# Performance work log

Hardware: AMD Instinct MI355X
Metric: run time of the kernel (lower is better)

The kernel has to match this reference:

```python
import jax, jax.numpy as jnp
import numpy as np

B, S, HID = 2, 2048, 2048
NH, NKV, HD = 16, 8, 256
EPS = 1e-6
SCALE = 256 ** -0.5  # query_pre_attn_scalar ** -0.5


def setup_inputs() -> dict:
    key = jax.random.key(0)
    k1, k2, k3 = jax.random.split(key, 3)
    hidden_states = jax.random.normal(k1, (B, S, HID), dtype=jnp.float32)
    w_qkv = jax.random.normal(k2, (HID, (NH + 2 * NKV) * HD), dtype=jnp.float32) * 0.02
    w_o = jax.random.normal(k3, (NH * HD, HID), dtype=jnp.float32) * 0.02
    q_norm_w = jnp.zeros((HD,), dtype=jnp.float32)  # Gemma RMSNorm uses (1 + w)
    k_norm_w = jnp.zeros((HD,), dtype=jnp.float32)
    # Real rotary tables: inv_freq over half dim, emb = concat(freqs, freqs)
    inv_freq = 1.0 / (10000.0 ** (jnp.arange(0, HD, 2, dtype=jnp.float32) / HD))
    pos = jnp.arange(S, dtype=jnp.float32)
    freqs = pos[:, None] * inv_freq[None, :]            # [S, HD/2]
    emb = jnp.concatenate([freqs, freqs], axis=-1)       # [S, HD]
    cos = jnp.broadcast_to(jnp.cos(emb)[None], (B, S, HD))
    sin = jnp.broadcast_to(jnp.sin(emb)[None], (B, S, HD))
    return {"hidden_states": hidden_states, "cos": cos, "sin": sin,
            "w_qkv": w_qkv, "w_o": w_o, "q_norm_w": q_norm_w, "k_norm_w": k_norm_w}


def _rms_norm(x, w):
    # Gemma3RMSNorm: fp32 rms, scale by (1 + w)
    xf = x.astype(jnp.float32)
    var = jnp.mean(xf * xf, axis=-1, keepdims=True)
    out = xf * jax.lax.rsqrt(var + EPS) * (1.0 + w.astype(jnp.float32))
    return out.astype(x.dtype)


def _rotate_half(x):
    x1, x2 = jnp.split(x, 2, axis=-1)
    return jnp.concatenate([-x2, x1], axis=-1)


def reference(hidden_states, cos, sin, w_qkv, w_o, q_norm_w, k_norm_w):
    qkv = jnp.einsum("bsh,hf->bsf", hidden_states, w_qkv)
    q, k, v = jnp.split(qkv, [NH * HD, NH * HD + NKV * HD], axis=-1)
    q = q.reshape(B, S, NH, HD).transpose(0, 2, 1, 3)    # [b, nh, s, d]
    k = k.reshape(B, S, NKV, HD).transpose(0, 2, 1, 3)   # [b, nkv, s, d]
    v = v.reshape(B, S, NKV, HD).transpose(0, 2, 1, 3)
    q = _rms_norm(q, q_norm_w)
    k = _rms_norm(k, k_norm_w)
    c = cos[:, None, :, :]  # broadcast over heads
    s = sin[:, None, :, :]
    q = q * c + _rotate_half(q) * s
    k = k * c + _rotate_half(k) * s
    n_rep = NH // NKV
    k = jnp.repeat(k, n_rep, axis=1)  # GQA expand: [b, nh, s, d]
    v = jnp.repeat(v, n_rep, axis=1)
    scores = jnp.einsum("bhqd,bhkd->bhqk", q, k) * SCALE
    attn = jax.nn.softmax(scores, axis=-1)
    out = jnp.einsum("bhqk,bhkd->bhqd", attn, v)
    out = out.transpose(0, 2, 1, 3).reshape(B, S, NH * HD)
    return jnp.einsum("bsf,fh->bsh", out, w_o)
```

## Files before the change

kernel.cpp:

```cpp
#include <hip/hip_runtime.h>
#include <stdint.h>

typedef __attribute__((ext_vector_type(8))) short short8;
typedef __attribute__((ext_vector_type(4))) short short4v;
typedef __attribute__((ext_vector_type(4))) float f32x4;

#define GLOAD16(gp, lp) __builtin_amdgcn_global_load_lds( \
    (__attribute__((address_space(1))) void*)(gp),        \
    (__attribute__((address_space(3))) void*)(lp), 16, 0, 0)

__device__ __forceinline__ unsigned short f2bf(float f) {
    union { float f; unsigned u; } v; v.f = f;
    unsigned u = v.u + 0x7fffu + ((v.u >> 16) & 1u);
    return (unsigned short)(u >> 16);
}
__device__ __forceinline__ float bf2f(short s) {
    union { unsigned u; float f; } v;
    v.u = ((unsigned)(unsigned short)s) << 16;
    return v.f;
}

__global__ __launch_bounds__(256) void cvt_f32_bf16(const float* __restrict__ in,
                                                    short* __restrict__ out) {
    const int i = (blockIdx.x * 256 + threadIdx.x) * 4;
    const float4 v = *(const float4*)(in + i);
    short4v o;
    o[0] = (short)f2bf(v.x); o[1] = (short)f2bf(v.y);
    o[2] = (short)f2bf(v.z); o[3] = (short)f2bf(v.w);
    *(short4v*)(out + i) = o;
}

__global__ __launch_bounds__(256) void transpose_cvt(const float* __restrict__ in,
                                                     short* __restrict__ out,
                                                     int R, int C) {
    __shared__ float tile[64 * 65];
    const int t = threadIdx.x;
    const int r0 = blockIdx.y * 64, c0 = blockIdx.x * 64;
    const int rl = t >> 4, cl4 = (t & 15) * 4;
#pragma unroll
    for (int rep = 0; rep < 4; rep++) {
        const int r = rep * 16 + rl;
        const float4 v = *(const float4*)(in + (long)(r0 + r) * C + c0 + cl4);
        tile[r * 65 + cl4 + 0] = v.x;
        tile[r * 65 + cl4 + 1] = v.y;
        tile[r * 65 + cl4 + 2] = v.z;
        tile[r * 65 + cl4 + 3] = v.w;
    }
    __syncthreads();
#pragma unroll
    for (int rep = 0; rep < 4; rep++) {
        const int cc = rep * 16 + rl;
        short4v o;
#pragma unroll
        for (int j = 0; j < 4; j++) o[j] = (short)f2bf(tile[(cl4 + j) * 65 + cc]);
        *(short4v*)(out + (long)(c0 + cc) * R + r0 + cl4) = o;
    }
}

__global__ __launch_bounds__(256) void vtrans(const short* __restrict__ QKV,
                                              short* __restrict__ Vt) {
    __shared__ short tile[64 * 72];
    const int t = threadIdx.x;
    const int s0 = blockIdx.x * 64, d0 = blockIdx.y * 64;
    const int hb = blockIdx.z >> 1, b = blockIdx.z & 1;
    const short* src = QKV + ((long)(24 + hb) * 4096 + b * 2048) * 256;
    short* dst = Vt + (long)blockIdx.z * 256 * 2048;
#pragma unroll
    for (int p = 0; p < 2; p++) {
        const int c = p * 256 + t;
        const int r = c >> 3, col8 = (c & 7) * 8;
        *(short8*)(tile + r * 72 + col8) = *(const short8*)(src + (long)(s0 + r) * 256 + d0 + col8);
    }
    __syncthreads();
#pragma unroll
    for (int p = 0; p < 2; p++) {
        const int c = p * 256 + t;
        const int dr = c >> 3, sc8 = (c & 7) * 8;
        short8 o;
#pragma unroll
        for (int j = 0; j < 8; j++) o[j] = tile[(sc8 + j) * 72 + dr];
        *(short8*)(dst + (long)(d0 + dr) * 2048 + s0 + sc8) = o;
    }
}

template<int N, int K, int OUTMODE>
__global__ __launch_bounds__(256) void gemm_nt(const short* __restrict__ A,
                                               const short* __restrict__ Bt,
                                               void* __restrict__ Cv) {
    __shared__ __align__(16) short Al[128 * 32];
    __shared__ __align__(16) short Bl[128 * 32];
    const int t = threadIdx.x;
    const int lane = t & 63, w = t >> 6;
    const int quad = lane >> 4, l16 = lane & 15;
    const int wr = w >> 1, wc = w & 1;
    const long m0 = (long)blockIdx.y * 128, n0 = (long)blockIdx.x * 128;

    const short* Ag0 = A + (m0 + (t >> 2)) * K + (t & 3) * 8;
    const short* Bg0 = Bt + (n0 + (t >> 2)) * K + (t & 3) * 8;

    f32x4 acc[4][4] = {};

    for (int k0 = 0; k0 < K; k0 += 32) {
        __syncthreads();
        GLOAD16(Ag0 + k0,            Al + t * 8);
        GLOAD16(Ag0 + 64 * K + k0,   Al + (t + 256) * 8);
        GLOAD16(Bg0 + k0,            Bl + t * 8);
        GLOAD16(Bg0 + 64 * K + k0,   Bl + (t + 256) * 8);
        __syncthreads();
        short8 af[4], bfr[4];
#pragma unroll
        for (int i = 0; i < 4; i++)
            af[i] = *(const short8*)(Al + (wr * 64 + i * 16 + l16) * 32 + quad * 8);
#pragma unroll
        for (int i = 0; i < 4; i++)
            bfr[i] = *(const short8*)(Bl + (wc * 64 + i * 16 + l16) * 32 + quad * 8);
#pragma unroll
        for (int mi = 0; mi < 4; mi++)
#pragma unroll
            for (int ni = 0; ni < 4; ni++)
                acc[mi][ni] = __builtin_amdgcn_mfma_f32_16x16x32_bf16(af[mi], bfr[ni], acc[mi][ni], 0, 0, 0);
    }

    const long crow = m0 + wr * 64 + quad * 4;
    const long ccol = n0 + wc * 64 + l16;
    if constexpr (OUTMODE == 0) {
        float* C = (float*)Cv;
#pragma unroll
        for (int mi = 0; mi < 4; mi++)
#pragma unroll
            for (int ni = 0; ni < 4; ni++)
#pragma unroll
                for (int r = 0; r < 4; r++)
                    C[(crow + mi * 16 + r) * N + ccol + ni * 16] = acc[mi][ni][r];
    } else {
        short* C = (short*)Cv;
#pragma unroll
        for (int mi = 0; mi < 4; mi++)
#pragma unroll
            for (int ni = 0; ni < 4; ni++)
#pragma unroll
                for (int r = 0; r < 4; r++) {
                    const long m = crow + mi * 16 + r;
                    const long f = ccol + ni * 16;
                    C[(f >> 8) * 1048576 + m * 256 + (f & 255)] = (short)f2bf(acc[mi][ni][r]);
                }
    }
}

__global__ __launch_bounds__(256) void prep_qk(short* __restrict__ QKV,
                                               const float* __restrict__ cosp,
                                               const float* __restrict__ sinp,
                                               const float* __restrict__ qw,
                                               const float* __restrict__ kw) {
    const int t = threadIdx.x, w = t >> 6, lane = t & 63;
    const int d4 = lane * 4;
    const float sgn = (lane < 32) ? -1.0f : 1.0f;
#pragma unroll
    for (int i = 0; i < 4; i++) {
        const int g = blockIdx.x * 16 + w * 4 + i;
        const int u = g >> 12, m = g & 4095;
        short* rowp = QKV + (long)g * 256;
        const short4v raw = *(const short4v*)(rowp + d4);
        float x[4];
#pragma unroll
        for (int j = 0; j < 4; j++) x[j] = bf2f(raw[j]);
        float ss = x[0]*x[0] + x[1]*x[1] + x[2]*x[2] + x[3]*x[3];
#pragma unroll
        for (int msk = 1; msk < 64; msk <<= 1) ss += __shfl_xor(ss, msk, 64);
        const float rinv = rsqrtf(ss * (1.0f / 256.0f) + 1e-6f);
        const float4 wv = *(const float4*)(((u < 16) ? qw : kw) + d4);
        const float wa[4] = {wv.x, wv.y, wv.z, wv.w};
        const float4 cv = *(const float4*)(cosp + (long)m * 256 + d4);
        const float4 sv = *(const float4*)(sinp + (long)m * 256 + d4);
        const float ca[4] = {cv.x, cv.y, cv.z, cv.w};
        const float sa[4] = {sv.x, sv.y, sv.z, sv.w};
        float n[4];
#pragma unroll
        for (int j = 0; j < 4; j++) n[j] = x[j] * rinv * (1.0f + wa[j]);
        const float scale = (u < 16) ? 0.0625f : 1.0f;
        short4v ov;
#pragma unroll
        for (int j = 0; j < 4; j++) {
            const float p = __shfl_xor(n[j], 32, 64);
            ov[j] = (short)f2bf((n[j] * ca[j] + sgn * p * sa[j]) * scale);
        }
        *(short4v*)(rowp + d4) = ov;
    }
}

__global__ __launch_bounds__(512, 2) void attn(const short* __restrict__ QKV,
                                               const short* __restrict__ Vt,
                                               short* __restrict__ O) {
    __shared__ __align__(16) short Kl[2][64 * 256];
    __shared__ __align__(16) short Vl[256 * 64];
    __shared__ __align__(16) short Pl[128 * 72];
    __shared__ __align__(16) float Alp[128];
    __shared__ __align__(16) float Ll[128];

    const int t = threadIdx.x, w = t >> 6, lane = t & 63;
    const int quad = lane >> 4, l16 = lane & 15;
    const int q0 = blockIdx.x * 128, h = blockIdx.y, b = blockIdx.z;
    const int kh = h >> 1;
    const short* Qp = QKV + ((long)h * 4096 + b * 2048 + q0) * 256;
    const short* Kp = QKV + ((long)(16 + kh) * 4096 + b * 2048) * 256;
    const short* Vp = Vt + (long)(kh * 2 + b) * 256 * 2048;

    short8 qf[8];
#pragma unroll
    for (int ks = 0; ks < 8; ks++)
        qf[ks] = *(const short8*)(Qp + (w * 16 + l16) * 256 + ks * 32 + quad * 8);

    f32x4 acc[4][4] = {};
    float mi_[4], li_[4];
#pragma unroll
    for (int r = 0; r < 4; r++) { mi_[r] = -1e30f; li_[r] = 0.0f; }

    const int qh = w >> 2, dstr = (w & 3) * 64;

#pragma unroll
    for (int i = 0; i < 4; i++) {
        const int c = i * 512 + t;
        const int rK = c >> 5, j = c & 31;
        GLOAD16(Kp + (long)rK * 256 + (j ^ (rK & 31)) * 8, Kl[0] + c * 8);
    }

    for (int kt = 0; kt < 32; kt++) {
        const int k0 = kt * 64;
        __syncthreads();

#pragma unroll
        for (int i = 0; i < 4; i++) {
            const int c = i * 512 + t;
            const int dV = c >> 3, j = c & 7;
            GLOAD16(Vp + (long)dV * 2048 + k0 + (j ^ (dV & 7)) * 8, Vl + c * 8);
        }
        const int kn = ((kt + 1) & 31) * 64;
#pragma unroll
        for (int i = 0; i < 4; i++) {
            const int c = i * 512 + t;
            const int rK = c >> 5, j = c & 31;
            GLOAD16(Kp + (long)(kn + rK) * 256 + (j ^ (rK & 31)) * 8, Kl[(kt + 1) & 1] + c * 8);
        }

        const short* Kb = Kl[kt & 1];
        f32x4 sc[4] = {};
#pragma unroll
        for (int ct = 0; ct < 4; ct++) {
            const int rowK = ct * 16 + l16;
#pragma unroll
            for (int ks = 0; ks < 8; ks++) {
                const int dc = (ks * 4 + quad) ^ (rowK & 31);
                const short8 kf = *(const short8*)(Kb + rowK * 256 + dc * 8);
                sc[ct] = __builtin_amdgcn_mfma_f32_16x16x32_bf16(qf[ks], kf, sc[ct], 0, 0, 0);
            }
        }

        float al[4];
#pragma unroll
        for (int r = 0; r < 4; r++) {
            float v = fmaxf(fmaxf(sc[0][r], sc[1][r]), fmaxf(sc[2][r], sc[3][r]));
            v = fmaxf(v, __shfl_xor(v, 1, 64));
            v = fmaxf(v, __shfl_xor(v, 2, 64));
            v = fmaxf(v, __shfl_xor(v, 4, 64));
            v = fmaxf(v, __shfl_xor(v, 8, 64));
            const float mn = fmaxf(mi_[r], v);
            al[r] = __expf(mi_[r] - mn);
            mi_[r] = mn;
        }
        float rs[4] = {0.0f, 0.0f, 0.0f, 0.0f};
#pragma unroll
        for (int ct = 0; ct < 4; ct++) {
#pragma unroll
            for (int r = 0; r < 4; r++) {
                const float p = __expf(sc[ct][r] - mi_[r]);
                rs[r] += p;
                Pl[(w * 16 + quad * 4 + r) * 72 + ct * 16 + l16] = (short)f2bf(p);
            }
        }
#pragma unroll
        for (int r = 0; r < 4; r++) {
            float v = rs[r];
            v += __shfl_xor(v, 1, 64);
            v += __shfl_xor(v, 2, 64);
            v += __shfl_xor(v, 4, 64);
            v += __shfl_xor(v, 8, 64);
            li_[r] = li_[r] * al[r] + v;
        }
        if (l16 == 0) {
#pragma unroll
            for (int r = 0; r < 4; r++) Alp[w * 16 + quad * 4 + r] = al[r];
        }
        __syncthreads();

#pragma unroll
        for (int mi2 = 0; mi2 < 4; mi2++) {
            const float4 av = *(const float4*)(Alp + qh * 64 + mi2 * 16 + quad * 4);
            const float aa[4] = {av.x, av.y, av.z, av.w};
#pragma unroll
            for (int ni = 0; ni < 4; ni++)
#pragma unroll
                for (int r = 0; r < 4; r++)
                    acc[mi2][ni][r] *= aa[r];
        }
#pragma unroll
        for (int k2 = 0; k2 < 2; k2++) {
            short8 pf[4];
#pragma unroll
            for (int mi2 = 0; mi2 < 4; mi2++)
                pf[mi2] = *(const short8*)(Pl + (qh * 64 + mi2 * 16 + l16) * 72 + k2 * 32 + quad * 8);
#pragma unroll
            for (int ni = 0; ni < 4; ni++) {
                const int dV = dstr + ni * 16 + l16;
                const int dc = (k2 * 4 + quad) ^ (dV & 7);
                const short8 vf = *(const short8*)(Vl + dV * 64 + dc * 8);
#pragma unroll
                for (int mi2 = 0; mi2 < 4; mi2++)
                    acc[mi2][ni] = __builtin_amdgcn_mfma_f32_16x16x32_bf16(pf[mi2], vf, acc[mi2][ni], 0, 0, 0);
            }
        }
    }

    if (l16 == 0) {
#pragma unroll
        for (int r = 0; r < 4; r++) Ll[w * 16 + quad * 4 + r] = li_[r];
    }
    __syncthreads();

    short* Op = O + (long)(b * 2048 + q0 + qh * 64) * 4096 + h * 256 + dstr;
#pragma unroll
    for (int mi2 = 0; mi2 < 4; mi2++) {
        const float4 lv = *(const float4*)(Ll + qh * 64 + mi2 * 16 + quad * 4);
        const float inv[4] = {1.0f / lv.x, 1.0f / lv.y, 1.0f / lv.z, 1.0f / lv.w};
#pragma unroll
        for (int ni = 0; ni < 4; ni++)
#pragma unroll
            for (int r = 0; r < 4; r++)
                Op[(long)(mi2 * 16 + quad * 4 + r) * 4096 + ni * 16 + l16] =
                    (short)f2bf(acc[mi2][ni][r] * inv[r]);
    }
}

extern "C" void kernel_launch(void* const* d_in, const int* in_sizes, int n_in,
                              void* d_out, int out_size, void* d_ws, size_t ws_size,
                              hipStream_t stream) {
    const float* hs   = (const float*)d_in[0];
    const float* cosp = (const float*)d_in[1];
    const float* sinp = (const float*)d_in[2];
    const float* wqkv = (const float*)d_in[3];
    const float* wo   = (const float*)d_in[4];
    const float* qnw  = (const float*)d_in[5];
    const float* knw  = (const float*)d_in[6];
    float* out = (float*)d_out;

    short* poolA  = (short*)d_ws;
    short* Xb     = poolA;
    short* Wqkv_t = poolA + (size_t)4096 * 2048;
    short* QKV    = poolA + (size_t)4096 * 2048 + (size_t)8192 * 2048;
    short* Vt     = poolA;
    short* Ob     = poolA + (size_t)16 * 256 * 2048;
    short* Wo_t   = QKV;

    cvt_f32_bf16<<<8192, 256, 0, stream>>>(hs, Xb);
    transpose_cvt<<<dim3(128, 32), 256, 0, stream>>>(wqkv, Wqkv_t, 2048, 8192);
    gemm_nt<8192, 2048, 2><<<dim3(64, 32), 256, 0, stream>>>(Xb, Wqkv_t, (void*)QKV);
    prep_qk<<<6144, 256, 0, stream>>>(QKV, cosp, sinp, qnw, knw);
    vtrans<<<dim3(32, 4, 16), 256, 0, stream>>>(QKV, Vt);
    attn<<<dim3(16, 16, 2), 512, 0, stream>>>(QKV, Vt, Ob);
    transpose_cvt<<<dim3(32, 64), 256, 0, stream>>>(wo, Wo_t, 4096, 2048);
    gemm_nt<2048, 4096, 0><<<dim3(16, 32), 256, 0, stream>>>(Ob, Wo_t, (void*)out);
}
```

Measured before the change: 674.1 us.

## Warp-specialize attention into QK-softmax and PV warps with software pipelining

Splits the eight waves of the attention block into four score waves, which compute QK^T and softmax for 32 query rows each, and four PV waves, which accumulate P·V for all 128 rows over a 64-column slice of the head dimension. V is double-buffered and the PV step runs one tile behind the score step, so the two phases overlap across iterations. This is meant to hide softmax latency behind MFMA work. The cost is a larger accumulator (128 fp32 values per lane in the PV waves), which adds register pressure and may reduce occupancy under launch_bounds(512,2), plus an extra 32 KB of LDS and one extra loop iteration.

```diff
diff --git a/kernel.cpp b/kernel.cpp
--- a/kernel.cpp
+++ b/kernel.cpp
@@ -192,7 +192,7 @@
                                                const short* __restrict__ Vt,
                                                short* __restrict__ O) {
     __shared__ __align__(16) short Kl[2][64 * 256];
-    __shared__ __align__(16) short Vl[256 * 64];
+    __shared__ __align__(16) short Vl[2][256 * 64];
     __shared__ __align__(16) short Pl[128 * 72];
     __shared__ __align__(16) float Alp[128];
     __shared__ __align__(16) float Ll[128];
@@ -205,17 +205,32 @@
     const short* Kp = QKV + ((long)(16 + kh) * 4096 + b * 2048) * 256;
     const short* Vp = Vt + (long)(kh * 2 + b) * 256 * 2048;
 
-    short8 qf[8];
-#pragma unroll
-    for (int ks = 0; ks < 8; ks++)
-        qf[ks] = *(const short8*)(Qp + (w * 16 + l16) * 256 + ks * 32 + quad * 8);
-
-    f32x4 acc[4][4] = {};
-    float mi_[4], li_[4];
-#pragma unroll
-    for (int r = 0; r < 4; r++) { mi_[r] = -1e30f; li_[r] = 0.0f; }
-
-    const int qh = w >> 2, dstr = (w & 3) * 64;
+    const bool is_s = (w < 4);
+    const int qb = w * 32;
+    const int dstr = (w - 4) * 64;
+
+    short8 qf[2][8];
+    f32x4 sc[2][4];
+    float mi_[2][4], li_[2][4];
+    f32x4 acc[8][4];
+
+    if (is_s) {
+#pragma unroll
+        for (int g = 0; g < 2; g++)
+#pragma unroll
+            for (int ks = 0; ks < 8; ks++)
+                qf[g][ks] = *(const short8*)(Qp + (qb + g * 16 + l16) * 256 + ks * 32 + quad * 8);
+#pragma unroll
+        for (int g = 0; g < 2; g++)
+#pragma unroll
+            for (int r = 0; r < 4; r++) { mi_[g][r] = -1e30f; li_[g][r] = 0.0f; }
+    } else {
+#pragma unroll
+        for (int qt = 0; qt < 8; qt++)
+#pragma unroll
+            for (int dt = 0; dt < 4; dt++)
+                acc[qt][dt] = (f32x4){0.f, 0.f, 0.f, 0.f};
+    }
 
 #pragma unroll
     for (int i = 0; i < 4; i++) {
@@ -224,119 +239,141 @@
         GLOAD16(Kp + (long)rK * 256 + (j ^ (rK & 31)) * 8, Kl[0] + c * 8);
     }
 
-    for (int kt = 0; kt < 32; kt++) {
-        const int k0 = kt * 64;
+    for (int kt = 0; kt <= 32; kt++) {
         __syncthreads();
 
-#pragma unroll
-        for (int i = 0; i < 4; i++) {
-            const int c = i * 512 + t;
-            const int dV = c >> 3, j = c & 7;
-            GLOAD16(Vp + (long)dV * 2048 + k0 + (j ^ (dV & 7)) * 8, Vl + c * 8);
-        }
-        const int kn = ((kt + 1) & 31) * 64;
-#pragma unroll
-        for (int i = 0; i < 4; i++) {
-            const int c = i * 512 + t;
-            const int rK = c >> 5, j = c & 31;
-            GLOAD16(Kp + (long)(kn + rK) * 256 + (j ^ (rK & 31)) * 8, Kl[(kt + 1) & 1] + c * 8);
-        }
-
-        const short* Kb = Kl[kt & 1];
-        f32x4 sc[4] = {};
-#pragma unroll
-        for (int ct = 0; ct < 4; ct++) {
-            const int rowK = ct * 16 + l16;
-#pragma unroll
-            for (int ks = 0; ks < 8; ks++) {
-                const int dc = (ks * 4 + quad) ^ (rowK & 31);
-                const short8 kf = *(const short8*)(Kb + rowK * 256 + dc * 8);
-                sc[ct] = __builtin_amdgcn_mfma_f32_16x16x32_bf16(qf[ks], kf, sc[ct], 0, 0, 0);
-            }
-        }
-
-        float al[4];
-#pragma unroll
-        for (int r = 0; r < 4; r++) {
-            float v = fmaxf(fmaxf(sc[0][r], sc[1][r]), fmaxf(sc[2][r], sc[3][r]));
-            v = fmaxf(v, __shfl_xor(v, 1, 64));
-            v = fmaxf(v, __shfl_xor(v, 2, 64));
-            v = fmaxf(v, __shfl_xor(v, 4, 64));
-            v = fmaxf(v, __shfl_xor(v, 8, 64));
-            const float mn = fmaxf(mi_[r], v);
-            al[r] = __expf(mi_[r] - mn);
-            mi_[r] = mn;
-        }
-        float rs[4] = {0.0f, 0.0f, 0.0f, 0.0f};
-#pragma unroll
-        for (int ct = 0; ct < 4; ct++) {
-#pragma unroll
-            for (int r = 0; r < 4; r++) {
-                const float p = __expf(sc[ct][r] - mi_[r]);
-                rs[r] += p;
-                Pl[(w * 16 + quad * 4 + r) * 72 + ct * 16 + l16] = (short)f2bf(p);
-            }
-        }
-#pragma unroll
-        for (int r = 0; r < 4; r++) {
-            float v = rs[r];
-            v += __shfl_xor(v, 1, 64);
-            v += __shfl_xor(v, 2, 64);
-            v += __shfl_xor(v, 4, 64);
-            v += __shfl_xor(v, 8, 64);
-            li_[r] = li_[r] * al[r] + v;
-        }
-        if (l16 == 0) {
-#pragma unroll
-            for (int r = 0; r < 4; r++) Alp[w * 16 + quad * 4 + r] = al[r];
-        }
+        if (kt < 32) {
+            const int k0 = kt * 64;
+#pragma unroll
+            for (int i = 0; i < 4; i++) {
+                const int c = i * 512 + t;
+                const int dV = c >> 3, j = c & 7;
+                GLOAD16(Vp + (long)dV * 2048 + k0 + (j ^ (dV & 7)) * 8, Vl[kt & 1] + c * 8);
+            }
+        }
+        if (kt + 1 < 32) {
+            const int kn = (kt + 1) * 64;
+#pragma unroll
+            for (int i = 0; i < 4; i++) {
+                const int c = i * 512 + t;
+                const int rK = c >> 5, j = c & 31;
+                GLOAD16(Kp + (long)(kn + rK) * 256 + (j ^ (rK & 31)) * 8, Kl[(kt + 1) & 1] + c * 8);
+            }
+        }
+
+        if (is_s) {
+            if (kt < 32) {
+                const short* Kb = Kl[kt & 1];
+#pragma unroll
+                for (int g = 0; g < 2; g++)
+#pragma unroll
+                    for (int ct = 0; ct < 4; ct++) sc[g][ct] = (f32x4){0.f, 0.f, 0.f, 0.f};
+#pragma unroll
+                for (int ct = 0; ct < 4; ct++) {
+                    const int rowK = ct * 16 + l16;
+#pragma unroll
+                    for (int ks = 0; ks < 8; ks++) {
+                        const int dc = (ks * 4 + quad) ^ (rowK & 31);
+                        const short8 kf = *(const short8*)(Kb + rowK * 256 + dc * 8);
+                        sc[0][ct] = __builtin_amdgcn_mfma_f32_16x16x32_bf16(qf[0][ks], kf, sc[0][ct], 0, 0, 0);
+                        sc[1][ct] = __builtin_amdgcn_mfma_f32_16x16x32_bf16(qf[1][ks], kf, sc[1][ct], 0, 0, 0);
+                    }
+                }
+            }
+        } else if (kt >= 1) {
+            const short* Vb = Vl[(kt - 1) & 1];
+#pragma unroll
+            for (int qt = 0; qt < 8; qt++) {
+                const float4 av = *(const float4*)(Alp + qt * 16 + quad * 4);
+                const float aa[4] = {av.x, av.y, av.z, av.w};
+#pragma unroll
+                for (int dt = 0; dt < 4; dt++)
+#pragma unroll
+                    for (int r = 0; r < 4; r++) acc[qt][dt][r] *= aa[r];
+            }
+#pragma unroll
+            for (int k2 = 0; k2 < 2; k2++) {
+                short8 vf[4];
+#pragma unroll
+                for (int dt = 0; dt < 4; dt++) {
+                    const int dV = dstr + dt * 16 + l16;
+                    const int dc = (k2 * 4 + quad) ^ (dV & 7);
+                    vf[dt] = *(const short8*)(Vb + dV * 64 + dc * 8);
+                }
+#pragma unroll
+                for (int qt = 0; qt < 8; qt++) {
+                    const short8 pf = *(const short8*)(Pl + (qt * 16 + l16) * 72 + k2 * 32 + quad * 8);
+#pragma unroll
+                    for (int dt = 0; dt < 4; dt++)
+                        acc[qt][dt] = __builtin_amdgcn_mfma_f32_16x16x32_bf16(pf, vf[dt], acc[qt][dt], 0, 0, 0);
+                }
+            }
+        }
+
         __syncthreads();
 
-#pragma unroll
-        for (int mi2 = 0; mi2 < 4; mi2++) {
-            const float4 av = *(const float4*)(Alp + qh * 64 + mi2 * 16 + quad * 4);
-            const float aa[4] = {av.x, av.y, av.z, av.w};
-#pragma unroll
-            for (int ni = 0; ni < 4; ni++)
+        if (is_s && kt < 32) {
+#pragma unroll
+            for (int g = 0; g < 2; g++) {
+                float al[4];
+#pragma unroll
+                for (int r = 0; r < 4; r++) {
+                    float v = fmaxf(fmaxf(sc[g][0][r], sc[g][1][r]), fmaxf(sc[g][2][r], sc[g][3][r]));
+                    v = fmaxf(v, __shfl_xor(v, 1, 64));
+                    v = fmaxf(v, __shfl_xor(v, 2, 64));
+                    v = fmaxf(v, __shfl_xor(v, 4, 64));
+                    v = fmaxf(v, __shfl_xor(v, 8, 64));
+                    const float mn = fmaxf(mi_[g][r], v);
+                    al[r] = __expf(mi_[g][r] - mn);
+                    mi_[g][r] = mn;
+                }
+                float rs[4] = {0.f, 0.f, 0.f, 0.f};
+#pragma unroll
+                for (int ct = 0; ct < 4; ct++) {
+#pragma unroll
+                    for (int r = 0; r < 4; r++) {
+                        const float p = __expf(sc[g][ct][r] - mi_[g][r]);
+                        rs[r] += p;
+                        Pl[(qb + g * 16 + quad * 4 + r) * 72 + ct * 16 + l16] = (short)f2bf(p);
+                    }
+                }
+#pragma unroll
+                for (int r = 0; r < 4; r++) {
+                    float v = rs[r];
+                    v += __shfl_xor(v, 1, 64);
+                    v += __shfl_xor(v, 2, 64);
+                    v += __shfl_xor(v, 4, 64);
+                    v += __shfl_xor(v, 8, 64);
+                    li_[g][r] = li_[g][r] * al[r] + v;
+                }
+                if (l16 == 0) {
+#pragma unroll
+                    for (int r = 0; r < 4; r++) Alp[qb + g * 16 + quad * 4 + r] = al[r];
+                }
+            }
+        }
+    }
+
+    if (is_s && l16 == 0) {
+#pragma unroll
+        for (int g = 0; g < 2; g++)
+#pragma unroll
+            for (int r = 0; r < 4; r++) Ll[qb + g * 16 + quad * 4 + r] = li_[g][r];
+    }
+    __syncthreads();
+    if (!is_s) {
+        short* Op = O + (long)(b * 2048 + q0) * 4096 + h * 256 + dstr;
+#pragma unroll
+        for (int qt = 0; qt < 8; qt++) {
+            const float4 lv = *(const float4*)(Ll + qt * 16 + quad * 4);
+            const float inv[4] = {1.0f / lv.x, 1.0f / lv.y, 1.0f / lv.z, 1.0f / lv.w};
+#pragma unroll
+            for (int dt = 0; dt < 4; dt++)
 #pragma unroll
                 for (int r = 0; r < 4; r++)
-                    acc[mi2][ni][r] *= aa[r];
-        }
-#pragma unroll
-        for (int k2 = 0; k2 < 2; k2++) {
-            short8 pf[4];
-#pragma unroll
-            for (int mi2 = 0; mi2 < 4; mi2++)
-                pf[mi2] = *(const short8*)(Pl + (qh * 64 + mi2 * 16 + l16) * 72 + k2 * 32 + quad * 8);
-#pragma unroll
-            for (int ni = 0; ni < 4; ni++) {
-                const int dV = dstr + ni * 16 + l16;
-                const int dc = (k2 * 4 + quad) ^ (dV & 7);
-                const short8 vf = *(const short8*)(Vl + dV * 64 + dc * 8);
-#pragma unroll
-                for (int mi2 = 0; mi2 < 4; mi2++)
-                    acc[mi2][ni] = __builtin_amdgcn_mfma_f32_16x16x32_bf16(pf[mi2], vf, acc[mi2][ni], 0, 0, 0);
-            }
-        }
-    }
-
-    if (l16 == 0) {
-#pragma unroll
-        for (int r = 0; r < 4; r++) Ll[w * 16 + quad * 4 + r] = li_[r];
-    }
-    __syncthreads();
-
-    short* Op = O + (long)(b * 2048 + q0 + qh * 64) * 4096 + h * 256 + dstr;
-#pragma unroll
-    for (int mi2 = 0; mi2 < 4; mi2++) {
-        const float4 lv = *(const float4*)(Ll + qh * 64 + mi2 * 16 + quad * 4);
-        const float inv[4] = {1.0f / lv.x, 1.0f / lv.y, 1.0f / lv.z, 1.0f / lv.w};
-#pragma unroll
-        for (int ni = 0; ni < 4; ni++)
-#pragma unroll
-            for (int r = 0; r < 4; r++)
-                Op[(long)(mi2 * 16 + quad * 4 + r) * 4096 + ni * 16 + l16] =
-                    (short)f2bf(acc[mi2][ni][r] * inv[r]);
+                    Op[(long)(qt * 16 + quad * 4 + r) * 4096 + dt * 16 + l16] =
+                        (short)f2bf(acc[qt][dt][r] * inv[r]);
+        }
     }
 }
 
```

Result: slower. 1.100 ms (+63.2%).
